# Optimization experiments

Hardware: AMD Instinct MI355X
Metric: run time of the kernel (lower is better)

## Reference

```python
import jax, jax.numpy as jnp
import numpy as np
from jax import lax

SEQ_LEN = 4096
INPUT_SIZE = 1024
HIDDEN = 1024
NUM_CLASSES = 3


def setup_inputs() -> dict:
    key = jax.random.key(0)
    ks = jax.random.split(key, 12)
    s = 1.0 / np.sqrt(HIDDEN)  # torch LSTM/Linear uniform init scale
    def u(k, shape):
        return jax.random.uniform(k, shape, jnp.float32, -s, s)
    inp = jax.random.normal(ks[0], (SEQ_LEN, 1, INPUT_SIZE), jnp.float32)
    return {
        "inp": inp,
        # forward-direction LSTM params (gate order i,f,g,o as in torch)
        "Wih_f": u(ks[1], (4 * HIDDEN, INPUT_SIZE)),
        "Whh_f": u(ks[2], (4 * HIDDEN, HIDDEN)),
        "bih_f": u(ks[3], (4 * HIDDEN,)),
        "bhh_f": u(ks[4], (4 * HIDDEN,)),
        # backward-direction LSTM params
        "Wih_b": u(ks[5], (4 * HIDDEN, INPUT_SIZE)),
        "Whh_b": u(ks[6], (4 * HIDDEN, HIDDEN)),
        "bih_b": u(ks[7], (4 * HIDDEN,)),
        "bhh_b": u(ks[8], (4 * HIDDEN,)),
        # output head: Linear(2*HIDDEN, 3)
        "W_ho": u(ks[9], (NUM_CLASSES, 2 * HIDDEN)),
        "b_ho": u(ks[10], (NUM_CLASSES,)),
    }


def _lstm_last_h(x, Wih, Whh, bih, bhh):
    # x: (T, B, I) -> final hidden state (B, H)
    H = Whh.shape[1]
    B = x.shape[1]
    bias = bih + bhh
    # precompute input projections for all timesteps: (T, B, 4H)
    xg = jnp.einsum('tbi,gi->tbg', x, Wih) + bias

    def step(carry, xt):
        h, c = carry
        gates = xt + h @ Whh.T  # (B, 4H)
        i, f, g, o = jnp.split(gates, 4, axis=-1)
        c = jax.nn.sigmoid(f) * c + jax.nn.sigmoid(i) * jnp.tanh(g)
        h = jax.nn.sigmoid(o) * jnp.tanh(c)
        return (h, c), None

    init = (jnp.zeros((B, H), x.dtype), jnp.zeros((B, H), x.dtype))
    (hT, _), _ = lax.scan(step, init, xg)
    return hT


def reference(inp, Wih_f, Whh_f, bih_f, bhh_f, Wih_b, Whh_b, bih_b, bhh_b, W_ho, b_ho):
    h_fwd = _lstm_last_h(inp, Wih_f, Whh_f, bih_f, bhh_f)          # (1, H)
    h_bwd = _lstm_last_h(inp[::-1], Wih_b, Whh_b, bih_b, bhh_b)    # (1, H)
    hidden = jnp.concatenate([h_fwd, h_bwd], axis=-1)              # (1, 2H)
    # Dropout(p=0.35) is identity in eval mode.
    return hidden @ W_ho.T + b_ho                                  # (1, 3)
```

## Files before the change

### kernel.cpp

```cpp
#include <hip/hip_runtime.h>
#include <stdint.h>


#define T_SEQ 4096
#define ISZ   1024
#define HID   1024
#define NB_TOT 256
#define NTHR  512
#define PAD   68

typedef unsigned long long u64;

__device__ __forceinline__ float fast_sigmoid(float x) {
    return 1.0f / (1.0f + __expf(-x));
}
__device__ __forceinline__ float fast_tanh(float x) {
    return 1.0f - 2.0f / (__expf(2.0f * x) + 1.0f);
}

#define PIN4(v) asm volatile("" : "+v"(v.x), "+v"(v.y), "+v"(v.z), "+v"(v.w))
#define DOT4(a, b) ((a).x*(b).x + (a).y*(b).y + (a).z*(b).z + (a).w*(b).w)

#define GM 64
#define GN 64
#define GK 32

__global__ __launch_bounds__(256)
void xproj_gemm(const float* __restrict__ x,
                const float* __restrict__ Wih_f, const float* __restrict__ bih_f,
                const float* __restrict__ bhh_f,
                const float* __restrict__ Wih_b, const float* __restrict__ bih_b,
                const float* __restrict__ bhh_b,
                float* __restrict__ xg)
{
    const int dir = blockIdx.z;
    const float* Wih = dir ? Wih_b : Wih_f;
    const float* bih = dir ? bih_b : bih_f;
    const float* bhh = dir ? bhh_b : bhh_f;
    const int m0 = blockIdx.y * GM;
    const int n0 = blockIdx.x * GN;
    const int tid = threadIdx.x;
    const int ms = tid >> 2;
    const int kq = tid & 3;
    const int tm = tid >> 4;
    const int tn = tid & 15;

    __shared__ float As[GK][GM + 4];
    __shared__ float Bs[GK][GN + 4];

    float acc[4][4] = {};

    const int mrow = m0 + ms;
    const int xrow = dir ? (T_SEQ - 1 - mrow) : mrow;
    const float* ap = x + (size_t)xrow * ISZ + kq * 8;
    const float* bp = Wih + (size_t)(n0 + ms) * ISZ + kq * 8;

    for (int k0 = 0; k0 < ISZ; k0 += GK) {
        float4 a0 = *(const float4*)(ap + k0);
        float4 a1 = *(const float4*)(ap + k0 + 4);
        float4 b0 = *(const float4*)(bp + k0);
        float4 b1 = *(const float4*)(bp + k0 + 4);
        __syncthreads();
        const int kb = kq * 8;
        As[kb+0][ms]=a0.x; As[kb+1][ms]=a0.y; As[kb+2][ms]=a0.z; As[kb+3][ms]=a0.w;
        As[kb+4][ms]=a1.x; As[kb+5][ms]=a1.y; As[kb+6][ms]=a1.z; As[kb+7][ms]=a1.w;
        Bs[kb+0][ms]=b0.x; Bs[kb+1][ms]=b0.y; Bs[kb+2][ms]=b0.z; Bs[kb+3][ms]=b0.w;
        Bs[kb+4][ms]=b1.x; Bs[kb+5][ms]=b1.y; Bs[kb+6][ms]=b1.z; Bs[kb+7][ms]=b1.w;
        __syncthreads();
        #pragma unroll
        for (int k = 0; k < GK; ++k) {
            float4 av = *(const float4*)&As[k][tm * 4];
            float4 bv = *(const float4*)&Bs[k][tn * 4];
            acc[0][0] += av.x*bv.x; acc[0][1] += av.x*bv.y; acc[0][2] += av.x*bv.z; acc[0][3] += av.x*bv.w;
            acc[1][0] += av.y*bv.x; acc[1][1] += av.y*bv.y; acc[1][2] += av.y*bv.z; acc[1][3] += av.y*bv.w;
            acc[2][0] += av.z*bv.x; acc[2][1] += av.z*bv.y; acc[2][2] += av.z*bv.z; acc[2][3] += av.z*bv.w;
            acc[3][0] += av.w*bv.x; acc[3][1] += av.w*bv.y; acc[3][2] += av.w*bv.z; acc[3][3] += av.w*bv.w;
        }
    }

    const int gc = n0 + tn * 4;
    float4 bb1 = *(const float4*)(bih + gc);
    float4 bb2 = *(const float4*)(bhh + gc);
    float bx = bb1.x + bb2.x, by = bb1.y + bb2.y, bz = bb1.z + bb2.z, bw = bb1.w + bb2.w;
    float* op = xg + ((size_t)dir << 24) + (size_t)(m0 + tm * 4) * 4096 + gc;
    #pragma unroll
    for (int i = 0; i < 4; ++i) {
        float4 v;
        v.x = acc[i][0] + bx; v.y = acc[i][1] + by;
        v.z = acc[i][2] + bz; v.w = acc[i][3] + bw;
        *(float4*)(op + (size_t)i * 4096) = v;
    }
}

__global__ __attribute__((amdgpu_flat_work_group_size(NTHR, NTHR)))
           __attribute__((amdgpu_waves_per_eu(2, 2)))
void bilstm_rec(const float* __restrict__ xg,
                const float* __restrict__ Whh_f, const float* __restrict__ Whh_b,
                u64* hpack)
{
    const int tid = threadIdx.x;
    const int blk = blockIdx.x;
    const int dir = blk >> 7;
    const int lb  = blk & 127;
    const int u0  = lb * 8;
    const int w   = tid >> 6;
    const int l   = tid & 63;
    const int q   = l >> 4;
    const int kc  = l & 15;
    const int unit = u0 + w;
    const int grow = q * HID + unit;

    const float* Whh = dir ? Whh_b : Whh_f;
    const float* xgd = xg + ((size_t)dir << 24);
    u64* hp = hpack + (size_t)dir * 2 * HID;

    __shared__ __align__(16) float lds_h[2][16 * PAD];

    const float* wp = Whh + (size_t)grow * HID + kc * 64;
    float4 w0 = *(const float4*)(wp + 0),  w1 = *(const float4*)(wp + 4);
    float4 w2 = *(const float4*)(wp + 8),  w3 = *(const float4*)(wp + 12);
    float4 w4 = *(const float4*)(wp + 16), w5 = *(const float4*)(wp + 20);
    float4 w6 = *(const float4*)(wp + 24), w7 = *(const float4*)(wp + 28);
    float4 w8 = *(const float4*)(wp + 32), w9 = *(const float4*)(wp + 36);
    float4 wa = *(const float4*)(wp + 40), wb = *(const float4*)(wp + 44);
    float4 wc = *(const float4*)(wp + 48), wd = *(const float4*)(wp + 52);
    float4 we = *(const float4*)(wp + 56), wf = *(const float4*)(wp + 60);
    PIN4(w0); PIN4(w1); PIN4(w2); PIN4(w3);
    PIN4(w4); PIN4(w5); PIN4(w6); PIN4(w7);
    PIN4(w8); PIN4(w9); PIN4(wa); PIN4(wb);
    PIN4(wc); PIN4(wd); PIN4(we); PIN4(wf);

    const float a_scl = (q == 2) ? 2.0f : 1.0f;
    const float a_mul = (q == 2) ? 2.0f : 1.0f;
    const float a_add = (q == 2) ? -1.0f : 0.0f;

    float c_state = 0.0f;
    float xgv = 0.0f;
    if (kc == 0) xgv = xgd[grow];
    asm volatile("" : "+v"(xgv));

    bool dead = false;

    for (int t = 0; t < T_SEQ; ++t) {
        float s = 0.0f;

        if (t > 0) {
            const int b = (t - 1) & 1;
            u64* src = hp + (size_t)b * HID;
            const int k0 = tid * 2;
            u64 e0 = 0, e1 = 0;
            if (!dead) {
                int sp = 0;
                for (;;) {
                    e0 = __hip_atomic_load(src + k0,     __ATOMIC_RELAXED,
                                           __HIP_MEMORY_SCOPE_AGENT);
                    e1 = __hip_atomic_load(src + k0 + 1, __ATOMIC_RELAXED,
                                           __HIP_MEMORY_SCOPE_AGENT);
                    if (((unsigned)(e0 >> 32) == (unsigned)t) &
                        ((unsigned)(e1 >> 32) == (unsigned)t)) break;
                    if (++sp > (1 << 21)) { dead = true; break; }
                    __builtin_amdgcn_s_sleep(1);
                }
            }
            float2 hv;
            hv.x = __uint_as_float((unsigned)(e0 & 0xffffffffu));
            hv.y = __uint_as_float((unsigned)(e1 & 0xffffffffu));
            *(float2*)&lds_h[b][(k0 >> 6) * PAD + (k0 & 63)] = hv;
            __syncthreads();

            const float* lh = &lds_h[b][kc * PAD];
            float4 h0 = *(const float4*)(lh + 0),  h1 = *(const float4*)(lh + 4);
            float4 h2 = *(const float4*)(lh + 8),  h3 = *(const float4*)(lh + 12);
            float4 h4 = *(const float4*)(lh + 16), h5 = *(const float4*)(lh + 20);
            float4 h6 = *(const float4*)(lh + 24), h7 = *(const float4*)(lh + 28);
            s  = DOT4(w0,h0) + DOT4(w1,h1) + DOT4(w2,h2) + DOT4(w3,h3);
            s += DOT4(w4,h4) + DOT4(w5,h5) + DOT4(w6,h6) + DOT4(w7,h7);
            float4 h8 = *(const float4*)(lh + 32), h9 = *(const float4*)(lh + 36);
            float4 ha = *(const float4*)(lh + 40), hb = *(const float4*)(lh + 44);
            float4 hc = *(const float4*)(lh + 48), hd = *(const float4*)(lh + 52);
            float4 he = *(const float4*)(lh + 56), hf = *(const float4*)(lh + 60);
            s += DOT4(w8,h8) + DOT4(w9,h9) + DOT4(wa,ha) + DOT4(wb,hb);
            s += DOT4(wc,hc) + DOT4(wd,hd) + DOT4(we,he) + DOT4(wf,hf);
        }

        s += __shfl_xor(s, 1);
        s += __shfl_xor(s, 2);
        s += __shfl_xor(s, 4);
        s += __shfl_xor(s, 8);

        float pg = s + xgv;
        float act = a_mul * fast_sigmoid(a_scl * pg) + a_add;

        float sf = __shfl(act, 16);
        float tg = __shfl(act, 32);
        float so = __shfl(act, 48);

        if (l == 0) {
            float si = act;
            c_state = sf * c_state + si * tg;
            float hval = so * fast_tanh(c_state);
            u64 pk = ((u64)(unsigned)(t + 1) << 32) | (u64)__float_as_uint(hval);
            __hip_atomic_store(hp + (size_t)(t & 1) * HID + unit, pk,
                               __ATOMIC_RELAXED, __HIP_MEMORY_SCOPE_AGENT);
        }

        if (t + 1 < T_SEQ && kc == 0) {
            xgv = xgd[(size_t)(t + 1) * 4096 + grow];
            asm volatile("" : "+v"(xgv));
        }
    }
}

__global__ void head_kernel(const float* __restrict__ W_ho,
                            const float* __restrict__ b_ho,
                            const u64* __restrict__ hpack,
                            float* __restrict__ out)
{
    const u64* hf  = hpack + 1 * HID;
    const u64* hbk = hpack + 2 * HID + 1 * HID;
    __shared__ float r0[4], r1[4], r2[4];
    int tid = threadIdx.x;
    float p0 = 0.f, p1 = 0.f, p2 = 0.f;
    for (int i = tid; i < 2 * HID; i += 256) {
        u64 e = (i < HID) ? hf[i] : hbk[i - HID];
        float hv = __uint_as_float((unsigned)(e & 0xffffffffu));
        p0 += W_ho[0 * 2 * HID + i] * hv;
        p1 += W_ho[1 * 2 * HID + i] * hv;
        p2 += W_ho[2 * 2 * HID + i] * hv;
    }
    #pragma unroll
    for (int m = 1; m < 64; m <<= 1) {
        p0 += __shfl_xor(p0, m);
        p1 += __shfl_xor(p1, m);
        p2 += __shfl_xor(p2, m);
    }
    int w = tid >> 6;
    if ((tid & 63) == 0) { r0[w] = p0; r1[w] = p1; r2[w] = p2; }
    __syncthreads();
    if (tid == 0) {
        out[0] = b_ho[0] + r0[0] + r0[1] + r0[2] + r0[3];
        out[1] = b_ho[1] + r1[0] + r1[1] + r1[2] + r1[3];
        out[2] = b_ho[2] + r2[0] + r2[1] + r2[2] + r2[3];
    }
}

extern "C" void kernel_launch(void* const* d_in, const int* in_sizes, int n_in,
                              void* d_out, int out_size, void* d_ws, size_t ws_size,
                              hipStream_t stream) {
    const float* x     = (const float*)d_in[0];
    const float* Wih_f = (const float*)d_in[1];
    const float* Whh_f = (const float*)d_in[2];
    const float* bih_f = (const float*)d_in[3];
    const float* bhh_f = (const float*)d_in[4];
    const float* Wih_b = (const float*)d_in[5];
    const float* Whh_b = (const float*)d_in[6];
    const float* bih_b = (const float*)d_in[7];
    const float* bhh_b = (const float*)d_in[8];
    const float* W_ho  = (const float*)d_in[9];
    const float* b_ho  = (const float*)d_in[10];

    u64* hpack = (u64*)d_ws;
    float* xg = (float*)((char*)d_ws + 32768);

    hipMemsetAsync(d_ws, 0, 2 * 2 * HID * sizeof(u64), stream);

    dim3 gg(4096 / GN, T_SEQ / GM, 2);
    xproj_gemm<<<gg, 256, 0, stream>>>(x, Wih_f, bih_f, bhh_f,
                                       Wih_b, bih_b, bhh_b, xg);
    bilstm_rec<<<NB_TOT, NTHR, 0, stream>>>(xg, Whh_f, Whh_b, hpack);
    head_kernel<<<1, 256, 0, stream>>>(W_ho, b_ho, hpack, (float*)d_out);
}
```

Baseline: 7.994 ms.

## Halve recurrent block count by assigning two hidden units per wave

The persistent recurrent kernel now runs 128 blocks instead of 256, and each wave computes two hidden units, keeping twice as many Whh weights resident in registers. The goal is to cut the number of blocks that poll and synchronize on the global h exchange at every timestep, which lowers the cost of the cross-block barrier in the serial recurrence. In exchange each wave doubles its register footprint (128 weight floats) and its per-step FMA work, which risks spilling under the 2-waves-per-EU bound and lengthening each step's critical path.

```diff
diff --git a/kernel.cpp b/kernel.cpp
--- a/kernel.cpp
+++ b/kernel.cpp
@@ -5,7 +5,7 @@
 #define T_SEQ 4096
 #define ISZ   1024
 #define HID   1024
-#define NB_TOT 256
+#define NB_TOT 128
 #define NTHR  512
 #define PAD   68
 
@@ -100,15 +100,15 @@
 {
     const int tid = threadIdx.x;
     const int blk = blockIdx.x;
-    const int dir = blk >> 7;
-    const int lb  = blk & 127;
-    const int u0  = lb * 8;
+    const int dir = blk >> 6;
+    const int lb  = blk & 63;
+    const int u0  = lb * 16;
     const int w   = tid >> 6;
     const int l   = tid & 63;
     const int q   = l >> 4;
     const int kc  = l & 15;
-    const int unit = u0 + w;
-    const int grow = q * HID + unit;
+    const int uA  = u0 + 2 * w;
+    const int growA = q * HID + uA;
 
     const float* Whh = dir ? Whh_b : Whh_f;
     const float* xgd = xg + ((size_t)dir << 24);
@@ -116,33 +116,49 @@
 
     __shared__ __align__(16) float lds_h[2][16 * PAD];
 
-    const float* wp = Whh + (size_t)grow * HID + kc * 64;
-    float4 w0 = *(const float4*)(wp + 0),  w1 = *(const float4*)(wp + 4);
-    float4 w2 = *(const float4*)(wp + 8),  w3 = *(const float4*)(wp + 12);
-    float4 w4 = *(const float4*)(wp + 16), w5 = *(const float4*)(wp + 20);
-    float4 w6 = *(const float4*)(wp + 24), w7 = *(const float4*)(wp + 28);
-    float4 w8 = *(const float4*)(wp + 32), w9 = *(const float4*)(wp + 36);
-    float4 wa = *(const float4*)(wp + 40), wb = *(const float4*)(wp + 44);
-    float4 wc = *(const float4*)(wp + 48), wd = *(const float4*)(wp + 52);
-    float4 we = *(const float4*)(wp + 56), wf = *(const float4*)(wp + 60);
-    PIN4(w0); PIN4(w1); PIN4(w2); PIN4(w3);
-    PIN4(w4); PIN4(w5); PIN4(w6); PIN4(w7);
-    PIN4(w8); PIN4(w9); PIN4(wa); PIN4(wb);
-    PIN4(wc); PIN4(wd); PIN4(we); PIN4(wf);
+    const float* wpA = Whh + (size_t)growA * HID + kc * 64;
+    const float* wpB = wpA + HID;
+    float4 a0 = *(const float4*)(wpA + 0),  a1 = *(const float4*)(wpA + 4);
+    float4 a2 = *(const float4*)(wpA + 8),  a3 = *(const float4*)(wpA + 12);
+    float4 a4 = *(const float4*)(wpA + 16), a5 = *(const float4*)(wpA + 20);
+    float4 a6 = *(const float4*)(wpA + 24), a7 = *(const float4*)(wpA + 28);
+    float4 a8 = *(const float4*)(wpA + 32), a9 = *(const float4*)(wpA + 36);
+    float4 aa = *(const float4*)(wpA + 40), ab = *(const float4*)(wpA + 44);
+    float4 ac = *(const float4*)(wpA + 48), ad = *(const float4*)(wpA + 52);
+    float4 ae = *(const float4*)(wpA + 56), af = *(const float4*)(wpA + 60);
+    float4 b0 = *(const float4*)(wpB + 0),  b1 = *(const float4*)(wpB + 4);
+    float4 b2 = *(const float4*)(wpB + 8),  b3 = *(const float4*)(wpB + 12);
+    float4 b4 = *(const float4*)(wpB + 16), b5 = *(const float4*)(wpB + 20);
+    float4 b6 = *(const float4*)(wpB + 24), b7 = *(const float4*)(wpB + 28);
+    float4 b8 = *(const float4*)(wpB + 32), b9 = *(const float4*)(wpB + 36);
+    float4 ba = *(const float4*)(wpB + 40), bb = *(const float4*)(wpB + 44);
+    float4 bc = *(const float4*)(wpB + 48), bd = *(const float4*)(wpB + 52);
+    float4 be = *(const float4*)(wpB + 56), bf = *(const float4*)(wpB + 60);
+    PIN4(a0); PIN4(a1); PIN4(a2); PIN4(a3);
+    PIN4(a4); PIN4(a5); PIN4(a6); PIN4(a7);
+    PIN4(a8); PIN4(a9); PIN4(aa); PIN4(ab);
+    PIN4(ac); PIN4(ad); PIN4(ae); PIN4(af);
+    PIN4(b0); PIN4(b1); PIN4(b2); PIN4(b3);
+    PIN4(b4); PIN4(b5); PIN4(b6); PIN4(b7);
+    PIN4(b8); PIN4(b9); PIN4(ba); PIN4(bb);
+    PIN4(bc); PIN4(bd); PIN4(be); PIN4(bf);
 
     const float a_scl = (q == 2) ? 2.0f : 1.0f;
     const float a_mul = (q == 2) ? 2.0f : 1.0f;
     const float a_add = (q == 2) ? -1.0f : 0.0f;
 
-    float c_state = 0.0f;
-    float xgv = 0.0f;
-    if (kc == 0) xgv = xgd[grow];
-    asm volatile("" : "+v"(xgv));
+    float cA = 0.0f, cB = 0.0f;
+    float xgvA = 0.0f, xgvB = 0.0f;
+    if (kc == 0) {
+        xgvA = xgd[growA];
+        xgvB = xgd[growA + 1];
+    }
+    asm volatile("" : "+v"(xgvA), "+v"(xgvB));
 
     bool dead = false;
 
     for (int t = 0; t < T_SEQ; ++t) {
-        float s = 0.0f;
+        float sA = 0.0f, sB = 0.0f;
 
         if (t > 0) {
             const int b = (t - 1) & 1;
@@ -173,40 +189,47 @@
             float4 h2 = *(const float4*)(lh + 8),  h3 = *(const float4*)(lh + 12);
             float4 h4 = *(const float4*)(lh + 16), h5 = *(const float4*)(lh + 20);
             float4 h6 = *(const float4*)(lh + 24), h7 = *(const float4*)(lh + 28);
-            s  = DOT4(w0,h0) + DOT4(w1,h1) + DOT4(w2,h2) + DOT4(w3,h3);
-            s += DOT4(w4,h4) + DOT4(w5,h5) + DOT4(w6,h6) + DOT4(w7,h7);
+            sA  = DOT4(a0,h0) + DOT4(a1,h1) + DOT4(a2,h2) + DOT4(a3,h3);
+            sA += DOT4(a4,h4) + DOT4(a5,h5) + DOT4(a6,h6) + DOT4(a7,h7);
+            sB  = DOT4(b0,h0) + DOT4(b1,h1) + DOT4(b2,h2) + DOT4(b3,h3);
+            sB += DOT4(b4,h4) + DOT4(b5,h5) + DOT4(b6,h6) + DOT4(b7,h7);
             float4 h8 = *(const float4*)(lh + 32), h9 = *(const float4*)(lh + 36);
             float4 ha = *(const float4*)(lh + 40), hb = *(const float4*)(lh + 44);
             float4 hc = *(const float4*)(lh + 48), hd = *(const float4*)(lh + 52);
             float4 he = *(const float4*)(lh + 56), hf = *(const float4*)(lh + 60);
-            s += DOT4(w8,h8) + DOT4(w9,h9) + DOT4(wa,ha) + DOT4(wb,hb);
-            s += DOT4(wc,hc) + DOT4(wd,hd) + DOT4(we,he) + DOT4(wf,hf);
-        }
-
-        s += __shfl_xor(s, 1);
-        s += __shfl_xor(s, 2);
-        s += __shfl_xor(s, 4);
-        s += __shfl_xor(s, 8);
-
-        float pg = s + xgv;
-        float act = a_mul * fast_sigmoid(a_scl * pg) + a_add;
-
-        float sf = __shfl(act, 16);
-        float tg = __shfl(act, 32);
-        float so = __shfl(act, 48);
+            sA += DOT4(a8,h8) + DOT4(a9,h9) + DOT4(aa,ha) + DOT4(ab,hb);
+            sA += DOT4(ac,hc) + DOT4(ad,hd) + DOT4(ae,he) + DOT4(af,hf);
+            sB += DOT4(b8,h8) + DOT4(b9,h9) + DOT4(ba,ha) + DOT4(bb,hb);
+            sB += DOT4(bc,hc) + DOT4(bd,hd) + DOT4(be,he) + DOT4(bf,hf);
+        }
+
+        sA += __shfl_xor(sA, 1);  sB += __shfl_xor(sB, 1);
+        sA += __shfl_xor(sA, 2);  sB += __shfl_xor(sB, 2);
+        sA += __shfl_xor(sA, 4);  sB += __shfl_xor(sB, 4);
+        sA += __shfl_xor(sA, 8);  sB += __shfl_xor(sB, 8);
+
+        float actA = a_mul * fast_sigmoid(a_scl * (sA + xgvA)) + a_add;
+        float actB = a_mul * fast_sigmoid(a_scl * (sB + xgvB)) + a_add;
+
+        float sfA = __shfl(actA, 16), tgA = __shfl(actA, 32), soA = __shfl(actA, 48);
+        float sfB = __shfl(actB, 16), tgB = __shfl(actB, 32), soB = __shfl(actB, 48);
 
         if (l == 0) {
-            float si = act;
-            c_state = sf * c_state + si * tg;
-            float hval = so * fast_tanh(c_state);
-            u64 pk = ((u64)(unsigned)(t + 1) << 32) | (u64)__float_as_uint(hval);
-            __hip_atomic_store(hp + (size_t)(t & 1) * HID + unit, pk,
-                               __ATOMIC_RELAXED, __HIP_MEMORY_SCOPE_AGENT);
+            cA = sfA * cA + actA * tgA;
+            float hA = soA * fast_tanh(cA);
+            cB = sfB * cB + actB * tgB;
+            float hB = soB * fast_tanh(cB);
+            u64 pkA = ((u64)(unsigned)(t + 1) << 32) | (u64)__float_as_uint(hA);
+            u64 pkB = ((u64)(unsigned)(t + 1) << 32) | (u64)__float_as_uint(hB);
+            u64* dst = hp + (size_t)(t & 1) * HID + uA;
+            __hip_atomic_store(dst,     pkA, __ATOMIC_RELAXED, __HIP_MEMORY_SCOPE_AGENT);
+            __hip_atomic_store(dst + 1, pkB, __ATOMIC_RELAXED, __HIP_MEMORY_SCOPE_AGENT);
         }
 
         if (t + 1 < T_SEQ && kc == 0) {
-            xgv = xgd[(size_t)(t + 1) * 4096 + grow];
-            asm volatile("" : "+v"(xgv));
+            xgvA = xgd[(size_t)(t + 1) * 4096 + growA];
+            xgvB = xgd[(size_t)(t + 1) * 4096 + growA + 1];
+            asm volatile("" : "+v"(xgvA), "+v"(xgvB));
         }
     }
 }
```

After: 9.233 ms. 1.16x slower.
